# Kernel tuning notes

Hardware: AMD Instinct MI355X
Metric: run time of the kernel (lower is better)

Reference implementation:

```python
import jax, jax.numpy as jnp
import numpy as np

D_MODEL = 256
N_HEADS = 8
D_FF = 1024
N_LAYERS = 6
INPUT_DIM = 2
EPS = 1e-5  # torch LayerNorm default


def _layer_norm(x, g, b):
    m = jnp.mean(x, axis=-1, keepdims=True)
    v = jnp.mean((x - m) ** 2, axis=-1, keepdims=True)
    return (x - m) / jnp.sqrt(v + EPS) * g + b


def setup_inputs() -> dict:
    key = jax.random.key(0)
    ks = jax.random.split(key, 8)
    f32 = jnp.float32

    def w(k, shape, fan_in):
        return jax.random.normal(k, shape, f32) * (1.0 / np.sqrt(fan_in))

    return {
        "x": jax.random.normal(ks[0], (8, 1024, INPUT_DIM), f32),
        "in_w": w(ks[1], (INPUT_DIM, D_MODEL), INPUT_DIM),
        "in_b": jnp.zeros((D_MODEL,), f32),
        "ln1_g": jnp.ones((D_MODEL,), f32),
        "ln1_b": jnp.zeros((D_MODEL,), f32),
        "qkv_w": w(ks[2], (D_MODEL, 3 * D_MODEL), D_MODEL),
        "qkv_b": jnp.zeros((3 * D_MODEL,), f32),
        "out_w": w(ks[3], (D_MODEL, D_MODEL), D_MODEL),
        "out_b": jnp.zeros((D_MODEL,), f32),
        "lna_g": jnp.ones((D_MODEL,), f32),
        "lna_b": jnp.zeros((D_MODEL,), f32),
        "ln2_g": jnp.ones((D_MODEL,), f32),
        "ln2_b": jnp.zeros((D_MODEL,), f32),
        "ff1_w": w(ks[4], (D_MODEL, D_FF), D_MODEL),
        "ff1_b": jnp.zeros((D_FF,), f32),
        "ff2_w": w(ks[5], (D_FF, D_MODEL), D_FF),
        "ff2_b": jnp.zeros((D_MODEL,), f32),
        "lnf_g": jnp.ones((D_MODEL,), f32),
        "lnf_b": jnp.zeros((D_MODEL,), f32),
    }


def reference(x, in_w, in_b, ln1_g, ln1_b, qkv_w, qkv_b, out_w, out_b,
              lna_g, lna_b, ln2_g, ln2_b, ff1_w, ff1_b, ff2_w, ff2_b,
              lnf_g, lnf_b):
    B, L, _ = x.shape
    dk = D_MODEL // N_HEADS
    scale = 1.0 / np.sqrt(dk)
    top_k = max(1, L // 4)

    # sinusoidal positional encoding [L, D]
    pos = jnp.arange(L, dtype=jnp.float32)[:, None]
    div = jnp.exp(jnp.arange(0, D_MODEL, 2, dtype=jnp.float32)
                  * (-np.log(10000.0) / D_MODEL))
    pe = jnp.zeros((L, D_MODEL), jnp.float32)
    pe = pe.at[:, 0::2].set(jnp.sin(pos * div))
    pe = pe.at[:, 1::2].set(jnp.cos(pos * div))

    h = x @ in_w + in_b + pe[None]  # [B, L, D]

    # VoformerEncoder reuses the SAME layer object -> shared weights, 6 passes
    for _ in range(N_LAYERS):
        # --- self-attention sublayer (pre-norm) ---
        s2 = _layer_norm(h, ln1_g, ln1_b)
        qkv = (s2 @ qkv_w + qkv_b).reshape(B, L, 3, N_HEADS, dk)
        q = qkv[:, :, 0].transpose(0, 2, 1, 3)  # [B, H, L, dk]
        k = qkv[:, :, 1].transpose(0, 2, 1, 3)
        v = qkv[:, :, 2].transpose(0, 2, 1, 3)

        scores = jnp.einsum('bhqd,bhkd->bhqk', q, k) * scale  # [B,H,L,L]
        # ProbSparse: keep only the per-row top-k scores
        thr = jax.lax.top_k(scores, top_k)[0][..., -1:]
        sparse = jnp.where(scores >= thr, scores, -jnp.inf)
        attn = jax.nn.softmax(sparse, axis=-1)
        o = jnp.einsum('bhqk,bhkd->bhqd', attn, v)
        o = o.transpose(0, 2, 1, 3).reshape(B, L, D_MODEL)
        o = o @ out_w + out_b
        # InformerAttention applies its own residual + LayerNorm
        attn_out = _layer_norm(o + s2, lna_g, lna_b)
        h = h + attn_out

        # --- FFN sublayer with Volatilite activation ---
        s2 = _layer_norm(h, ln2_g, ln2_b)
        f = s2 @ ff1_w + ff1_b  # [B, L, d_ff]
        mean_f = jnp.mean(f, axis=1, keepdims=True)
        vol = jnp.sqrt(jnp.mean((mean_f - f) ** 2, axis=1, keepdims=True))
        f = f * vol
        f = f @ ff2_w + ff2_b
        h = h + f

    return _layer_norm(h, lnf_g, lnf_b)
```

## Files before the change

kernel.cpp:

```cpp
#include <hip/hip_runtime.h>
#include <hip/hip_bf16.h>
#include <math.h>

#define D_MODEL 256
#define NH 8
#define DFF 1024
#define NLAYERS 6
#define B_ 8
#define L_ 1024
#define NR (B_*L_)
#define TOPK 256
#define LNEPS 1e-5f

typedef __attribute__((ext_vector_type(8))) short bf16x8;
typedef __attribute__((ext_vector_type(4))) float f32x4;

__device__ __forceinline__ float wsum(float v){
  #pragma unroll
  for(int o=32;o>0;o>>=1) v += __shfl_xor(v,o,64);
  return v;
}
__device__ __forceinline__ short f2bf(float x){
  unsigned u = __float_as_uint(x);
  u += 0x7fffu + ((u>>16)&1u);
  return (short)(u>>16);
}
__device__ __forceinline__ float bf2f(short s){
  return __uint_as_float(((unsigned)(unsigned short)s)<<16);
}
__device__ __forceinline__ unsigned pk2bf(float a, float b){
  __hip_bfloat162 h = __float22bfloat162_rn(make_float2(a,b));
  unsigned u; __builtin_memcpy(&u, &h, 4);
  return u;
}
__device__ __forceinline__ float kinvf(int k){
  unsigned u = (k & 0x8000) ? ((unsigned)k ^ 0x8000u) : ((unsigned)k ^ 0xFFFFu);
  return __uint_as_float(u << 16);
}
__device__ __forceinline__ void g2l(const short* g, short* l){
  __builtin_amdgcn_global_load_lds(
      (const __attribute__((address_space(1))) unsigned int*)g,
      (__attribute__((address_space(3))) unsigned int*)l,
      16, 0, 0);
}

__global__ __launch_bounds__(256) void embed_kernel(
    const float* __restrict__ x, const float* __restrict__ in_w,
    const float* __restrict__ in_b, float* __restrict__ h)
{
  int tid = blockIdx.x*256 + threadIdx.x;
  int n  = tid >> 6;
  int d0 = (tid & 63) << 2;
  int l  = n & (L_-1);
  float x0 = x[2*n], x1 = x[2*n+1];
  const float kf = -0.07195578415606394f;
  float pe[4];
  #pragma unroll
  for(int ii=0; ii<2; ++ii){
    int i = (d0>>1) + ii;
    float dv  = expf((float)i * kf);
    float ang = (float)l * dv;
    pe[2*ii]   = sinf(ang);
    pe[2*ii+1] = cosf(ang);
  }
  float4 w0 = *(const float4*)(in_w + d0);
  float4 w1 = *(const float4*)(in_w + D_MODEL + d0);
  float4 bb = *(const float4*)(in_b + d0);
  float4 o;
  o.x = x0*w0.x + x1*w1.x + bb.x + pe[0];
  o.y = x0*w0.y + x1*w1.y + bb.y + pe[1];
  o.z = x0*w0.z + x1*w1.z + bb.z + pe[2];
  o.w = x0*w0.w + x1*w1.w + bb.w + pe[3];
  *(float4*)(h + (size_t)n*D_MODEL + d0) = o;
}

__global__ __launch_bounds__(256) void wcvt(
    const float* __restrict__ W, short* __restrict__ WT, int N, int kshift)
{
  int idx = blockIdx.x*256 + threadIdx.x;
  int K = 1<<kshift;
  if (idx >= N*K) return;
  int n = idx >> kshift, k = idx & (K-1);
  WT[idx] = f2bf(W[(size_t)k*N + n]);
}

template<int OM>
__global__ __launch_bounds__(256) void ln_kernel(
    const float* __restrict__ in, const float* __restrict__ g,
    const float* __restrict__ b, float* __restrict__ out,
    short* __restrict__ outb)
{
  int wave = threadIdx.x >> 6, lane = threadIdx.x & 63;
  int row = blockIdx.x*4 + wave;
  float4 v = ((const float4*)(in + (size_t)row*D_MODEL))[lane];
  float s  = v.x+v.y+v.z+v.w;
  float sq = v.x*v.x+v.y*v.y+v.z*v.z+v.w*v.w;
  s = wsum(s); sq = wsum(sq);
  float mean = s*(1.f/D_MODEL);
  float var  = sq*(1.f/D_MODEL) - mean*mean;
  float rstd = 1.f/sqrtf(var + LNEPS);
  float4 gv = ((const float4*)g)[lane];
  float4 bv = ((const float4*)b)[lane];
  float4 o;
  o.x = (v.x-mean)*rstd*gv.x + bv.x;
  o.y = (v.y-mean)*rstd*gv.y + bv.y;
  o.z = (v.z-mean)*rstd*gv.z + bv.z;
  o.w = (v.w-mean)*rstd*gv.w + bv.w;
  if (OM == 0){
    ((float4*)(out + (size_t)row*D_MODEL))[lane] = o;
  }
  if (OM == 2){
    uint2 pk; pk.x = pk2bf(o.x, o.y); pk.y = pk2bf(o.z, o.w);
    *(uint2*)(outb + (size_t)row*D_MODEL + lane*4) = pk;
  }
}

__global__ __launch_bounds__(256) void lnln_kernel(
    const float* __restrict__ tb,
    const float* __restrict__ ga, const float* __restrict__ ba,
    const float* __restrict__ g2, const float* __restrict__ b2,
    float* __restrict__ h, short* __restrict__ s2b)
{
  int wave = threadIdx.x >> 6, lane = threadIdx.x & 63;
  int row = blockIdx.x*4 + wave;
  float4 v = ((const float4*)(tb + (size_t)row*D_MODEL))[lane];
  float s  = v.x+v.y+v.z+v.w;
  float sq = v.x*v.x+v.y*v.y+v.z*v.z+v.w*v.w;
  s = wsum(s); sq = wsum(sq);
  float mean = s*(1.f/D_MODEL);
  float var  = sq*(1.f/D_MODEL) - mean*mean;
  float rstd = 1.f/sqrtf(var + LNEPS);
  float4 gv = ((const float4*)ga)[lane];
  float4 bv = ((const float4*)ba)[lane];
  float4* hp = (float4*)(h + (size_t)row*D_MODEL) + lane;
  float4 hv = *hp;
  float4 hn;
  hn.x = hv.x + (v.x-mean)*rstd*gv.x + bv.x;
  hn.y = hv.y + (v.y-mean)*rstd*gv.y + bv.y;
  hn.z = hv.z + (v.z-mean)*rstd*gv.z + bv.z;
  hn.w = hv.w + (v.w-mean)*rstd*gv.w + bv.w;
  *hp = hn;
  float s2  = hn.x+hn.y+hn.z+hn.w;
  float sq2 = hn.x*hn.x+hn.y*hn.y+hn.z*hn.z+hn.w*hn.w;
  s2 = wsum(s2); sq2 = wsum(sq2);
  float m2 = s2*(1.f/D_MODEL);
  float v2 = sq2*(1.f/D_MODEL) - m2*m2;
  float r2 = 1.f/sqrtf(v2 + LNEPS);
  float4 g2v = ((const float4*)g2)[lane];
  float4 b2v = ((const float4*)b2)[lane];
  uint2 pk;
  pk.x = pk2bf((hn.x-m2)*r2*g2v.x + b2v.x, (hn.y-m2)*r2*g2v.y + b2v.y);
  pk.y = pk2bf((hn.z-m2)*r2*g2v.z + b2v.z, (hn.w-m2)*r2*g2v.w + b2v.w);
  *(uint2*)(s2b + (size_t)row*D_MODEL + lane*4) = pk;
}

template<int MODE>
__global__ __launch_bounds__(256) void mfma_gemm(
    const short* __restrict__ A, const short* __restrict__ BT,
    const float* __restrict__ bias, const short* __restrict__ residb,
    float* __restrict__ Cf, short* __restrict__ Cb, short* __restrict__ Vt,
    int N, int K)
{
  __shared__ __align__(16) short As[128*32];
  __shared__ __align__(16) short Bs[64*32];
  const int t = threadIdx.x, wv = t>>6, lane = t&63;
  const int r16 = lane&15, quad = lane>>4;
  const int m0 = blockIdx.y*128, n0 = blockIdx.x*64;
  const int ia0 = wv*128 + lane, ia1 = ia0 + 64;
  const int ib  = wv*64 + lane;
  const short* Ab = A  + (size_t)m0*K;
  const short* Bb = BT + (size_t)n0*K;
  const f32x4 z = {0.f,0.f,0.f,0.f};
  f32x4 acc[2][4];
  #pragma unroll
  for (int i=0;i<2;++i)
    #pragma unroll
    for (int j=0;j<4;++j) acc[i][j] = z;

  for (int k0 = 0; k0 < K; k0 += 32){
    __syncthreads();
    g2l(Ab + (size_t)(ia0>>2)*K + k0 + (ia0&3)*8, As + ia0*8);
    g2l(Ab + (size_t)(ia1>>2)*K + k0 + (ia1&3)*8, As + ia1*8);
    g2l(Bb + (size_t)(ib>>2)*K  + k0 + (ib&3)*8,  Bs + ib*8);
    __syncthreads();
    bf16x8 af0 = *(const bf16x8*)(As + ((wv*32      + r16)*32 + quad*8));
    bf16x8 af1 = *(const bf16x8*)(As + ((wv*32 + 16 + r16)*32 + quad*8));
    bf16x8 bf[4];
    #pragma unroll
    for (int ct=0; ct<4; ++ct)
      bf[ct] = *(const bf16x8*)(Bs + ((ct*16 + r16)*32 + quad*8));
    #pragma unroll
    for (int ct=0; ct<4; ++ct){
      acc[0][ct] = __builtin_amdgcn_mfma_f32_16x16x32_bf16(af0, bf[ct], acc[0][ct], 0,0,0);
      acc[1][ct] = __builtin_amdgcn_mfma_f32_16x16x32_bf16(af1, bf[ct], acc[1][ct], 0,0,0);
    }
  }

  #pragma unroll
  for (int rt=0; rt<2; ++rt){
    const int mb = m0 + wv*32 + rt*16 + quad*4;
    #pragma unroll
    for (int ct=0; ct<4; ++ct){
      const int n = n0 + ct*16 + r16;
      const float bv = bias[n];
      if (MODE == 0){
        if (n < 512){
          int region = n>>8, hh = (n>>5)&7, d = n&31;
          #pragma unroll
          for (int r=0;r<4;++r){
            int l = mb + r;
            size_t base = (((size_t)(region*64 + (l>>10)*8 + hh))*1024 + (l&1023))*32 + d;
            Cb[base] = f2bf(acc[rt][ct][r] + bv);
          }
        } else {
          int dv = n - 512, hh = dv>>5, d = dv&31;
          int b = mb>>10, lloc = mb&1023;
          size_t base = (((size_t)(b*8 + hh))*32 + d)*1024 + lloc;
          uint2 pk;
          pk.x = pk2bf(acc[rt][ct][0] + bv, acc[rt][ct][1] + bv);
          pk.y = pk2bf(acc[rt][ct][2] + bv, acc[rt][ct][3] + bv);
          *(uint2*)(Vt + base) = pk;
        }
      } else {
        #pragma unroll
        for (int r=0;r<4;++r){
          size_t off = (size_t)(mb + r)*N + n;
          float c = acc[rt][ct][r] + bv;
          if (MODE == 1) Cf[off] = c + bf2f(residb[off]);
          if (MODE == 2) Cb[off] = f2bf(c);
          if (MODE == 3) Cf[off] += c;
        }
      }
    }
  }
}

__global__ __launch_bounds__(512,8) void attn_mfma(
    const short* __restrict__ qkbf, const short* __restrict__ vT,
    short* __restrict__ ob)
{
  __shared__ __align__(16) short sc16[16*1024];
  __shared__ __align__(16) float po[8*256];
  const int t = threadIdx.x, wv = t>>6, lane = t&63;
  const int r16 = lane&15, quad = lane>>4;
  const int blk = blockIdx.x;
  const int bh = (blk & 7)*8 + ((blk>>3)&7);
  const int qt = blk >> 6;

  bf16x8 aq = *(const bf16x8*)(qkbf + ((size_t)bh*1024 + qt*16 + r16)*32 + quad*8);
  const short* kb = qkbf + (size_t)(64 + bh)*1024*32;
  short* p0 = sc16 + quad*4096;

  #pragma unroll
  for (int g=0; g<2; ++g){
    bf16x8 bkb[4];
    #pragma unroll
    for (int j=0;j<4;++j)
      bkb[j] = *(const bf16x8*)(kb + (size_t)(wv*128 + (g*4+j)*16 + r16)*32 + quad*8);
    #pragma unroll
    for (int j=0;j<4;++j){
      f32x4 c = {0.f,0.f,0.f,0.f};
      c = __builtin_amdgcn_mfma_f32_16x16x32_bf16(aq, bkb[j], c, 0, 0, 0);
      const int keyq = (wv*128 + (g*4+j)*16 + r16) ^ ((quad&1)<<5);
      unsigned u01 = pk2bf(c[0], c[1]);
      unsigned u23 = pk2bf(c[2], c[3]);
      p0[keyq]               = (short)u01;
      p0[1024 + (keyq ^ 8)]  = (short)(u01>>16);
      p0[2048 + (keyq ^ 16)] = (short)u23;
      p0[3072 + (keyq ^ 24)] = (short)(u23>>16);
    }
  }
  __syncthreads();

  const float SC2 = 0.25500529485087056f;
  {
    const int ra = wv*2;
    const int sa = (ra&7)<<3;
    short* pa = sc16 + ra*1024 + ((2*lane) ^ sa);
    short* pb = sc16 + (ra+1)*1024 + (((2*lane) ^ sa) ^ 8);
    float fa[16], fb[16];
    #pragma unroll
    for (int i=0;i<8;++i){
      unsigned wa = *(const unsigned*)(pa + i*128);
      unsigned wb = *(const unsigned*)(pb + i*128);
      fa[2*i]   = __uint_as_float(wa << 16);
      fa[2*i+1] = __uint_as_float(wa & 0xFFFF0000u);
      fb[2*i]   = __uint_as_float(wb << 16);
      fb[2*i+1] = __uint_as_float(wb & 0xFFFF0000u);
    }
    int loA = 0, loB = 0;
    #pragma unroll
    for (int bit = 15; bit >= 0; --bit){
      const int mA = loA | (1<<bit);
      const int mB = loB | (1<<bit);
      const float tA = kinvf(mA);
      const float tB = kinvf(mB);
      int cA = 0, cB = 0;
      #pragma unroll
      for (int i=0;i<16;++i){
        cA += (int)__popcll(__ballot(fa[i] >= tA));
        cB += (int)__popcll(__ballot(fb[i] >= tB));
      }
      if (cA >= TOPK) loA = mA;
      if (cB >= TOPK) loB = mB;
    }
    const float thrA = kinvf(loA), thrB = kinvf(loB);
    float ea[16], eb[16];
    float suma = 0.f, sumb = 0.f;
    #pragma unroll
    for (int i=0;i<16;++i){
      ea[i] = (fa[i] >= thrA) ? exp2f(fa[i]*SC2) : 0.f;
      eb[i] = (fb[i] >= thrB) ? exp2f(fb[i]*SC2) : 0.f;
      suma += ea[i]; sumb += eb[i];
    }
    suma = wsum(suma); sumb = wsum(sumb);
    const float inva = 1.f/suma, invb = 1.f/sumb;
    #pragma unroll
    for (int i=0;i<8;++i){
      *(unsigned*)(pa + i*128) = pk2bf(ea[2*i]*inva, ea[2*i+1]*inva);
      *(unsigned*)(pb + i*128) = pk2bf(eb[2*i]*invb, eb[2*i+1]*invb);
    }
  }
  __syncthreads();

  const int dh = wv>>2, ks = (wv&3)*256;
  const short* vb = vT + (size_t)bh*32*1024 + (size_t)(dh*16 + r16)*1024;
  const int sA = (r16&7) << 3;
  f32x4 oa = {0.f,0.f,0.f,0.f};
  #pragma unroll
  for (int j=0;j<8;++j){
    int k0 = ks + j*32;
    bf16x8 bv = *(const bf16x8*)(vb + k0 + quad*8);
    bf16x8 af = *(const bf16x8*)(sc16 + r16*1024 + ((k0 + quad*8) ^ sA));
    oa = __builtin_amdgcn_mfma_f32_16x16x32_bf16(af, bv, oa, 0, 0, 0);
  }
  #pragma unroll
  for (int r=0;r<4;++r)
    po[wv*256 + (quad*4+r)*16 + r16] = oa[r];
  __syncthreads();
  if (t < 256){
    int q = t>>4, d = (t&15)*2;
    int h4 = (d>>4)*4;
    float v0 = 0.f, v1 = 0.f;
    #pragma unroll
    for (int w=0;w<4;++w){
      v0 += po[(h4+w)*256 + q*16 + (d&15)];
      v1 += po[(h4+w)*256 + q*16 + ((d+1)&15)];
    }
    int b = bh>>3, hh = bh&7;
    size_t off = ((size_t)(b*1024 + qt*16 + q))*256 + hh*32 + d;
    *(unsigned*)(ob + off) = pk2bf(v0, v1);
  }
}

__global__ __launch_bounds__(512) void vol_scale(short* __restrict__ f)
{
  __shared__ float ps[8][64], pq[8][64], vs[64];
  int b = blockIdx.x >> 4, cb = blockIdx.x & 15;
  int cl = threadIdx.x & 63, sl = threadIdx.x >> 6;
  int col = cb*64 + cl;
  short* fb = f + (size_t)b*L_*DFF + col;
  float s = 0.f, sq = 0.f;
  for (int l = sl*128; l < sl*128+128; ++l){
    float v = bf2f(fb[(size_t)l*DFF]);
    s += v; sq += v*v;
  }
  ps[sl][cl] = s; pq[sl][cl] = sq;
  __syncthreads();
  if (threadIdx.x < 64){
    float st=0.f, qt=0.f;
    #pragma unroll
    for (int i=0;i<8;++i){ st += ps[i][cl]; qt += pq[i][cl]; }
    float mean = st*(1.f/L_);
    float var  = qt*(1.f/L_) - mean*mean;
    vs[cl] = sqrtf(fmaxf(var, 0.f));
  }
  __syncthreads();
  float vv = vs[cl];
  for (int l = sl*128; l < sl*128+128; ++l){
    size_t o = (size_t)l*DFF;
    fb[o] = f2bf(bf2f(fb[o]) * vv);
  }
}

extern "C" void kernel_launch(void* const* d_in, const int* in_sizes, int n_in,
                              void* d_out, int out_size, void* d_ws, size_t ws_size,
                              hipStream_t stream) {
  const float* x     = (const float*)d_in[0];
  const float* in_w  = (const float*)d_in[1];
  const float* in_b  = (const float*)d_in[2];
  const float* ln1_g = (const float*)d_in[3];
  const float* ln1_b = (const float*)d_in[4];
  const float* qkv_w = (const float*)d_in[5];
  const float* qkv_b = (const float*)d_in[6];
  const float* out_w = (const float*)d_in[7];
  const float* out_b = (const float*)d_in[8];
  const float* lna_g = (const float*)d_in[9];
  const float* lna_b = (const float*)d_in[10];
  const float* ln2_g = (const float*)d_in[11];
  const float* ln2_b = (const float*)d_in[12];
  const float* ff1_w = (const float*)d_in[13];
  const float* ff1_b = (const float*)d_in[14];
  const float* ff2_w = (const float*)d_in[15];
  const float* ff2_b = (const float*)d_in[16];
  const float* lnf_g = (const float*)d_in[17];
  const float* lnf_b = (const float*)d_in[18];
  float* out = (float*)d_out;

  char* ws = (char*)d_ws;
  float* h     = (float*)(ws);
  short* s2b   = (short*)(ws + (size_t)( 8<<20));
  short* qkbf  = (short*)(ws + (size_t)(12<<20));
  short* vTb   = (short*)(ws + (size_t)(20<<20));
  short* ob_b  = (short*)(ws + (size_t)(24<<20));
  short* f     = (short*)(ws + (size_t)(12<<20));
  float* tb    = (float*)(ws + (size_t)(28<<20));
  short* qkvwT = (short*)(ws + (size_t)(36<<20));
  short* outwT = (short*)(ws + (size_t)(36<<20) + 393216);
  short* ff1wT = (short*)(ws + (size_t)(36<<20) + 393216 + 131072);
  short* ff2wT = (short*)(ws + (size_t)(36<<20) + 393216 + 131072 + 524288);

  embed_kernel<<<NR*64/256, 256, 0, stream>>>(x, in_w, in_b, h);
  wcvt<<< 768, 256, 0, stream>>>(qkv_w, qkvwT,  768, 8);
  wcvt<<< 256, 256, 0, stream>>>(out_w, outwT,  256, 8);
  wcvt<<<1024, 256, 0, stream>>>(ff1_w, ff1wT, 1024, 8);
  wcvt<<<1024, 256, 0, stream>>>(ff2_w, ff2wT,  256, 10);

  for (int layer = 0; layer < NLAYERS; ++layer){
    ln_kernel<2><<<NR/4, 256, 0, stream>>>(h, ln1_g, ln1_b, nullptr, s2b);
    {
      dim3 g(768/64, NR/128);
      mfma_gemm<0><<<g, 256, 0, stream>>>(s2b, qkvwT, qkv_b, nullptr,
                                          nullptr, qkbf, vTb, 768, 256);
    }
    attn_mfma<<<64*64, 512, 0, stream>>>(qkbf, vTb, ob_b);
    {
      dim3 g(256/64, NR/128);
      mfma_gemm<1><<<g, 256, 0, stream>>>(ob_b, outwT, out_b, s2b,
                                          tb, nullptr, nullptr, 256, 256);
    }
    lnln_kernel<<<NR/4, 256, 0, stream>>>(tb, lna_g, lna_b, ln2_g, ln2_b, h, s2b);
    {
      dim3 g(1024/64, NR/128);
      mfma_gemm<2><<<g, 256, 0, stream>>>(s2b, ff1wT, ff1_b, nullptr,
                                          nullptr, f, nullptr, 1024, 256);
    }
    vol_scale<<<B_*16, 512, 0, stream>>>(f);
    {
      dim3 g(256/64, NR/128);
      mfma_gemm<3><<<g, 256, 0, stream>>>(f, ff2wT, ff2_b, nullptr,
                                          h, nullptr, nullptr, 256, 1024);
    }
  }
  ln_kernel<0><<<NR/4, 256, 0, stream>>>(h, lnf_g, lnf_b, out, nullptr);
}
```

Baseline: 1.166 ms.

## Store out-proj result as bf16, merge weight conversions, tweak attention LDS

Several unrelated tweaks. The output-projection GEMM now writes its residual sum as bf16 instead of fp32, and the LayerNorm kernel that follows reads bf16, halving that intermediate's traffic at the cost of extra rounding before the attention LayerNorm. The four weight-conversion launches become one kernel. The attention kernel makes the top-k threshold wave-uniform via readfirstlane and swizzles the partial-output LDS buffer so the reduction can use float2 reads with fewer bank conflicts.

```diff
diff --git a/kernel.cpp b/kernel.cpp
--- a/kernel.cpp
+++ b/kernel.cpp
@@ -74,12 +74,20 @@
   *(float4*)(h + (size_t)n*D_MODEL + d0) = o;
 }
 
-__global__ __launch_bounds__(256) void wcvt(
-    const float* __restrict__ W, short* __restrict__ WT, int N, int kshift)
-{
-  int idx = blockIdx.x*256 + threadIdx.x;
+__global__ __launch_bounds__(256) void wcvt_all(
+    const float* __restrict__ qkv_w, const float* __restrict__ out_w,
+    const float* __restrict__ ff1_w, const float* __restrict__ ff2_w,
+    short* __restrict__ qkvwT, short* __restrict__ outwT,
+    short* __restrict__ ff1wT, short* __restrict__ ff2wT)
+{
+  const int bid = blockIdx.x;
+  const float* W; short* WT; int N, kshift, base;
+  if (bid < 768)      { W=qkv_w; WT=qkvwT; N=768;  kshift=8;  base=0; }
+  else if (bid < 1024){ W=out_w; WT=outwT; N=256;  kshift=8;  base=768; }
+  else if (bid < 2048){ W=ff1_w; WT=ff1wT; N=1024; kshift=8;  base=1024; }
+  else                { W=ff2_w; WT=ff2wT; N=256;  kshift=10; base=2048; }
+  int idx = (bid-base)*256 + threadIdx.x;
   int K = 1<<kshift;
-  if (idx >= N*K) return;
   int n = idx >> kshift, k = idx & (K-1);
   WT[idx] = f2bf(W[(size_t)k*N + n]);
 }
@@ -116,14 +124,19 @@
 }
 
 __global__ __launch_bounds__(256) void lnln_kernel(
-    const float* __restrict__ tb,
+    const short* __restrict__ tbb,
     const float* __restrict__ ga, const float* __restrict__ ba,
     const float* __restrict__ g2, const float* __restrict__ b2,
     float* __restrict__ h, short* __restrict__ s2b)
 {
   int wave = threadIdx.x >> 6, lane = threadIdx.x & 63;
   int row = blockIdx.x*4 + wave;
-  float4 v = ((const float4*)(tb + (size_t)row*D_MODEL))[lane];
+  uint2 w = *(const uint2*)(tbb + (size_t)row*D_MODEL + lane*4);
+  float4 v;
+  v.x = __uint_as_float(w.x << 16);
+  v.y = __uint_as_float(w.x & 0xFFFF0000u);
+  v.z = __uint_as_float(w.y << 16);
+  v.w = __uint_as_float(w.y & 0xFFFF0000u);
   float s  = v.x+v.y+v.z+v.w;
   float sq = v.x*v.x+v.y*v.y+v.z*v.z+v.w*v.w;
   s = wsum(s); sq = wsum(sq);
@@ -226,7 +239,7 @@
         for (int r=0;r<4;++r){
           size_t off = (size_t)(mb + r)*N + n;
           float c = acc[rt][ct][r] + bv;
-          if (MODE == 1) Cf[off] = c + bf2f(residb[off]);
+          if (MODE == 1) Cb[off] = f2bf(c + bf2f(residb[off]));
           if (MODE == 2) Cb[off] = f2bf(c);
           if (MODE == 3) Cf[off] += c;
         }
@@ -293,8 +306,10 @@
     for (int bit = 15; bit >= 0; --bit){
       const int mA = loA | (1<<bit);
       const int mB = loB | (1<<bit);
-      const float tA = kinvf(mA);
-      const float tB = kinvf(mB);
+      const float tA = __uint_as_float(
+          __builtin_amdgcn_readfirstlane(__float_as_uint(kinvf(mA))));
+      const float tB = __uint_as_float(
+          __builtin_amdgcn_readfirstlane(__float_as_uint(kinvf(mB))));
       int cA = 0, cB = 0;
       #pragma unroll
       for (int i=0;i<16;++i){
@@ -335,17 +350,20 @@
     oa = __builtin_amdgcn_mfma_f32_16x16x32_bf16(af, bv, oa, 0, 0, 0);
   }
   #pragma unroll
-  for (int r=0;r<4;++r)
-    po[wv*256 + (quad*4+r)*16 + r16] = oa[r];
+  for (int r=0;r<4;++r){
+    int row = quad*4 + r;
+    po[wv*256 + ((row*16 + r16) ^ ((quad&1)<<4))] = oa[r];
+  }
   __syncthreads();
   if (t < 256){
     int q = t>>4, d = (t&15)*2;
     int h4 = (d>>4)*4;
+    int idx = (q*16 + (d&15)) ^ (((q>>2)&1)<<4);
     float v0 = 0.f, v1 = 0.f;
     #pragma unroll
     for (int w=0;w<4;++w){
-      v0 += po[(h4+w)*256 + q*16 + (d&15)];
-      v1 += po[(h4+w)*256 + q*16 + ((d+1)&15)];
+      float2 p = *(const float2*)(po + (h4+w)*256 + idx);
+      v0 += p.x; v1 += p.y;
     }
     int b = bh>>3, hh = bh&7;
     size_t off = ((size_t)(b*1024 + qt*16 + q))*256 + hh*32 + d;
@@ -414,17 +432,15 @@
   short* vTb   = (short*)(ws + (size_t)(20<<20));
   short* ob_b  = (short*)(ws + (size_t)(24<<20));
   short* f     = (short*)(ws + (size_t)(12<<20));
-  float* tb    = (float*)(ws + (size_t)(28<<20));
+  short* tbb   = (short*)(ws + (size_t)(28<<20));
   short* qkvwT = (short*)(ws + (size_t)(36<<20));
   short* outwT = (short*)(ws + (size_t)(36<<20) + 393216);
   short* ff1wT = (short*)(ws + (size_t)(36<<20) + 393216 + 131072);
   short* ff2wT = (short*)(ws + (size_t)(36<<20) + 393216 + 131072 + 524288);
 
   embed_kernel<<<NR*64/256, 256, 0, stream>>>(x, in_w, in_b, h);
-  wcvt<<< 768, 256, 0, stream>>>(qkv_w, qkvwT,  768, 8);
-  wcvt<<< 256, 256, 0, stream>>>(out_w, outwT,  256, 8);
-  wcvt<<<1024, 256, 0, stream>>>(ff1_w, ff1wT, 1024, 8);
-  wcvt<<<1024, 256, 0, stream>>>(ff2_w, ff2wT,  256, 10);
+  wcvt_all<<<3072, 256, 0, stream>>>(qkv_w, out_w, ff1_w, ff2_w,
+                                     qkvwT, outwT, ff1wT, ff2wT);
 
   for (int layer = 0; layer < NLAYERS; ++layer){
     ln_kernel<2><<<NR/4, 256, 0, stream>>>(h, ln1_g, ln1_b, nullptr, s2b);
@@ -437,9 +453,9 @@
     {
       dim3 g(256/64, NR/128);
       mfma_gemm<1><<<g, 256, 0, stream>>>(ob_b, outwT, out_b, s2b,
-                                          tb, nullptr, nullptr, 256, 256);
-    }
-    lnln_kernel<<<NR/4, 256, 0, stream>>>(tb, lna_g, lna_b, ln2_g, ln2_b, h, s2b);
+                                          nullptr, tbb, nullptr, 256, 256);
+    }
+    lnln_kernel<<<NR/4, 256, 0, stream>>>(tbb, lna_g, lna_b, ln2_g, ln2_b, h, s2b);
     {
       dim3 g(1024/64, NR/128);
       mfma_gemm<2><<<g, 256, 0, stream>>>(s2b, ff1wT, ff1_b, nullptr,
```

New measurement: 1.156 ms. No clear change (-0.8%).
